# Performance work log

Measured on AMD Instinct MI355X. Metric: run time of the kernel, lower is better.

## Reference

```python
import jax, jax.numpy as jnp
import numpy as np

NUM_HEADS = 16
ROPE_BASE = 10000.0


def _rope_tables(seq_len, head_dim, dtype=jnp.float32):
    # Standard RoPE: inv_freq over even dims, cos/sin of shape [seq, head_dim]
    inv_freq = 1.0 / (ROPE_BASE ** (jnp.arange(0, head_dim, 2, dtype=jnp.float32) / head_dim))
    freqs = jnp.arange(seq_len, dtype=jnp.float32)[:, None] * inv_freq[None, :]  # [S, hd/2]
    emb = jnp.concatenate([freqs, freqs], axis=-1)  # [S, hd]
    return jnp.cos(emb).astype(dtype), jnp.sin(emb).astype(dtype)


def _apply_rope(t, cos, sin):
    # t: [B, H, S, hd]; cos/sin: [S, hd]
    half = t.shape[-1] // 2
    rot = jnp.concatenate([-t[..., half:], t[..., :half]], axis=-1)
    return t * cos[None, None, :, :] + rot * sin[None, None, :, :]


def setup_inputs() -> dict:
    key = jax.random.key(0)
    ks = jax.random.split(key, 7)
    B, S, D, L = 2, 2048, 2048, 256
    sc = lambda fan_in: 1.0 / np.sqrt(fan_in)
    return {
        "x": jax.random.normal(ks[0], (B, S, D), jnp.float32),
        "wq": jax.random.normal(ks[1], (D, D), jnp.float32) * sc(D),
        "wdkv": jax.random.normal(ks[2], (L, D), jnp.float32) * sc(D),
        "wuk": jax.random.normal(ks[3], (D, L), jnp.float32) * sc(L),
        "wuv": jax.random.normal(ks[4], (D, L), jnp.float32) * sc(L),
        "wo": jax.random.normal(ks[5], (D, D), jnp.float32) * sc(D),
        "bo": jnp.zeros((D,), jnp.float32),
    }


def reference(x, wq, wdkv, wuk, wuv, wo, bo):
    B, S, D = x.shape
    H = NUM_HEADS
    hd = wq.shape[0] // H

    # Projections (torch nn.Linear: y = x @ W.T)
    q = jnp.einsum("bsd,ed->bse", x, wq)          # [B, S, D]
    latent = jnp.einsum("bsd,ld->bsl", x, wdkv)   # [B, S, L]
    k = jnp.einsum("bsl,el->bse", latent, wuk)    # [B, S, D]
    v = jnp.einsum("bsl,el->bse", latent, wuv)    # [B, S, D]

    split = lambda t: t.reshape(B, S, H, hd).transpose(0, 2, 1, 3)  # [B, H, S, hd]
    q, k, v = split(q), split(k), split(v)

    cos, sin = _rope_tables(S, hd, x.dtype)
    q = _apply_rope(q, cos, sin)
    k = _apply_rope(k, cos, sin)

    scores = jnp.einsum("bhqd,bhkd->bhqk", q, k) / jnp.sqrt(jnp.asarray(hd, x.dtype))
    causal = jnp.tril(jnp.ones((S, S), bool))
    scores = jnp.where(causal[None, None], scores, jnp.asarray(-jnp.inf, x.dtype))
    attn = jax.nn.softmax(scores, axis=-1)

    ctx = jnp.einsum("bhqk,bhkd->bhqd", attn, v)
    ctx = ctx.transpose(0, 2, 1, 3).reshape(B, S, H * hd)
    return jnp.einsum("bse,oe->bso", ctx, wo) + bo
```

## Files before the change

### kernel.cpp

```cpp
#include <hip/hip_runtime.h>
#include <hip/hip_bf16.h>

typedef __bf16 bf16;
typedef __bf16 bf16x8 __attribute__((ext_vector_type(8)));
typedef __bf16 bf16x4 __attribute__((ext_vector_type(4)));
typedef float  f32x4  __attribute__((ext_vector_type(4)));
typedef float  f32x16 __attribute__((ext_vector_type(16)));
typedef unsigned int u32x4 __attribute__((ext_vector_type(4)));

#define D_MODEL 2048
#define SEQ     2048
#define BATCH   2
#define NHEAD   16
#define HDIM    128
#define LATENT  256
#define BROWS   SEQ

typedef __attribute__((address_space(1))) void gvoid;
typedef __attribute__((address_space(3))) void svoid;

__device__ __forceinline__ void gld16(const bf16* g, bf16* l) {
  __builtin_amdgcn_global_load_lds((gvoid*)(void*)g, (svoid*)l, 16, 0, 0);
}

__device__ __forceinline__ f32x4 mfma16(bf16x8 a, bf16x8 b, f32x4 c) {
  return __builtin_amdgcn_mfma_f32_16x16x32_bf16(a, b, c, 0, 0, 0);
}
__device__ __forceinline__ f32x16 mfma32(bf16x8 a, bf16x8 b, f32x16 c) {
  return __builtin_amdgcn_mfma_f32_32x32x16_bf16(a, b, c, 0, 0, 0);
}

__device__ __forceinline__ unsigned cvt_pk_bf16(float lo, float hi) {
  unsigned r;
  asm("v_cvt_pk_bf16_f32 %0, %1, %2" : "=v"(r) : "v"(lo), "v"(hi));
  return r;
}

__device__ __forceinline__ float fw(float v) {
  union { float f; unsigned u; } x; x.f = v;
  if ((x.u & 0x7f800000u) == 0x7f800000u) return 0.f;
  return v;
}

template<typename T>
__device__ __forceinline__ bf16x8 ld_cvt8(const T* p);
template<>
__device__ __forceinline__ bf16x8 ld_cvt8<float>(const float* p) {
  const float4 a = *(const float4*)p;
  const float4 b = *(const float4*)(p + 4);
  bf16x8 r;
  r[0] = (bf16)a.x; r[1] = (bf16)a.y; r[2] = (bf16)a.z; r[3] = (bf16)a.w;
  r[4] = (bf16)b.x; r[5] = (bf16)b.y; r[6] = (bf16)b.z; r[7] = (bf16)b.w;
  return r;
}
template<>
__device__ __forceinline__ bf16x8 ld_cvt8<bf16>(const bf16* p) {
  return *(const bf16x8*)p;
}

template<typename TC>
__device__ __forceinline__ void st_c(TC* p, float v);
template<> __device__ __forceinline__ void st_c<bf16>(bf16* p, float v)   { *p = (bf16)v; }
template<> __device__ __forceinline__ void st_c<float>(float* p, float v) { *p = v; }

__global__ __launch_bounds__(256)
void cvt_bf16(const float* __restrict__ in, bf16* __restrict__ out, int n8)
{
  int i = blockIdx.x * 256 + threadIdx.x;
  if (i >= n8) return;
  const float4 a = ((const float4*)in)[2 * i];
  const float4 b = ((const float4*)in)[2 * i + 1];
  bf16x8 r;
  r[0] = (bf16)a.x; r[1] = (bf16)a.y; r[2] = (bf16)a.z; r[3] = (bf16)a.w;
  r[4] = (bf16)b.x; r[5] = (bf16)b.y; r[6] = (bf16)b.z; r[7] = (bf16)b.w;
  ((bf16x8*)out)[i] = r;
}

template<typename TA, typename TW, typename TC, int BIAS, int TRANSC>
__global__ __launch_bounds__(256)
void gemm_nt(const TA* __restrict__ A, const TW* __restrict__ W,
             TC* __restrict__ C, const float* __restrict__ bias,
             int M, int N, int K)
{
  const int t    = threadIdx.x;
  const int wave = t >> 6, lane = t & 63;
  const int quad = lane >> 4, l16 = lane & 15;
  const int wr = (wave >> 1) * 64, wc = (wave & 1) * 64;
  const int am0 = blockIdx.x * 128;
  const int bn0 = blockIdx.y * 128;

  __shared__ __align__(16) bf16 As[128][40];
  __shared__ __align__(16) bf16 Bs[128][40];

  const f32x4 fzero = {0.f, 0.f, 0.f, 0.f};
  f32x4 acc[4][4];
#pragma unroll
  for (int i = 0; i < 4; i++)
#pragma unroll
    for (int j = 0; j < 4; j++) acc[i][j] = fzero;

  const int srow = t >> 2;
  const int scol = (t & 3) * 8;

  for (int k0 = 0; k0 < K; k0 += 32) {
#pragma unroll
    for (int c = 0; c < 2; c++) {
      int row = srow + c * 64;
      *(bf16x8*)(&As[row][scol]) =
        ld_cvt8<TA>(A + (size_t)(am0 + row) * K + k0 + scol);
      *(bf16x8*)(&Bs[row][scol]) =
        ld_cvt8<TW>(W + (size_t)(bn0 + row) * K + k0 + scol);
    }
    __syncthreads();

    bf16x8 af[4], bfr[4];
#pragma unroll
    for (int i = 0; i < 4; i++)
      af[i]  = *(const bf16x8*)(&As[wr + i*16 + l16][quad*8]);
#pragma unroll
    for (int j = 0; j < 4; j++)
      bfr[j] = *(const bf16x8*)(&Bs[wc + j*16 + l16][quad*8]);
#pragma unroll
    for (int i = 0; i < 4; i++)
#pragma unroll
      for (int j = 0; j < 4; j++)
        acc[i][j] = mfma16(af[i], bfr[j], acc[i][j]);
    __syncthreads();
  }

#pragma unroll
  for (int i = 0; i < 4; i++) {
#pragma unroll
    for (int j = 0; j < 4; j++) {
      int col = bn0 + wc + j*16 + l16;
      float bv = 0.f;
      if (BIAS) bv = bias[col];
#pragma unroll
      for (int r = 0; r < 4; r++) {
        int row = am0 + wr + i*16 + quad*4 + r;
        if (TRANSC)
          st_c<TC>(&C[(size_t)col * M + row], fw(acc[i][j][r] + bv));
        else
          st_c<TC>(&C[(size_t)row * N + col], fw(acc[i][j][r] + bv));
      }
    }
  }
}

template<typename TC, int BIAS, int TRANSC>
__global__ __launch_bounds__(256)
void gemm_bb(const bf16* __restrict__ A, const bf16* __restrict__ W,
             TC* __restrict__ C, const float* __restrict__ bias,
             int M, int N, int K)
{
  const int t    = threadIdx.x;
  const int wave = t >> 6, lane = t & 63;
  const int quad = lane >> 4, l16 = lane & 15;
  const int wr = (wave >> 1) * 64, wc = (wave & 1) * 64;
  const int am0 = blockIdx.x * 128;
  const int bn0 = blockIdx.y * 128;

  __shared__ __align__(16) bf16 As[128 * 32];
  __shared__ __align__(16) bf16 Bs[128 * 32];

  const f32x4 fzero = {0.f, 0.f, 0.f, 0.f};
  f32x4 acc[4][4];
#pragma unroll
  for (int i = 0; i < 4; i++)
#pragma unroll
    for (int j = 0; j < 4; j++) acc[i][j] = fzero;

  for (int k0 = 0; k0 < K; k0 += 32) {
#pragma unroll
    for (int c = 0; c < 2; c++) {
      int e   = c * 256 + t;
      int row = e >> 2, col = (e & 3) * 8;
      gld16(A + (size_t)(am0 + row) * K + k0 + col, As + e * 8);
      gld16(W + (size_t)(bn0 + row) * K + k0 + col, Bs + e * 8);
    }
    __syncthreads();

    bf16x8 af[4], bfr[4];
#pragma unroll
    for (int i = 0; i < 4; i++)
      af[i]  = *(const bf16x8*)(As + (size_t)(wr + i*16 + l16) * 32 + quad * 8);
#pragma unroll
    for (int j = 0; j < 4; j++)
      bfr[j] = *(const bf16x8*)(Bs + (size_t)(wc + j*16 + l16) * 32 + quad * 8);
#pragma unroll
    for (int i = 0; i < 4; i++)
#pragma unroll
      for (int j = 0; j < 4; j++)
        acc[i][j] = mfma16(af[i], bfr[j], acc[i][j]);
    __syncthreads();
  }

#pragma unroll
  for (int i = 0; i < 4; i++) {
#pragma unroll
    for (int j = 0; j < 4; j++) {
      int col = bn0 + wc + j*16 + l16;
      float bv = 0.f;
      if (BIAS) bv = bias[col];
#pragma unroll
      for (int r = 0; r < 4; r++) {
        int row = am0 + wr + i*16 + quad*4 + r;
        if (TRANSC)
          st_c<TC>(&C[(size_t)col * M + row], fw(acc[i][j][r] + bv));
        else
          st_c<TC>(&C[(size_t)row * N + col], fw(acc[i][j][r] + bv));
      }
    }
  }
}

template<typename TC, int BIAS, int TRANSC>
__global__ __launch_bounds__(256)
void gemm_bf(const bf16* __restrict__ A, const float* __restrict__ W,
             TC* __restrict__ C, const float* __restrict__ bias,
             int M, int N, int K)
{
  const int t    = threadIdx.x;
  const int wave = t >> 6, lane = t & 63;
  const int quad = lane >> 4, l16 = lane & 15;
  const int wr = (wave >> 1) * 64, wc = (wave & 1) * 64;
  const int am0 = blockIdx.x * 128;
  const int bn0 = blockIdx.y * 128;

  __shared__ __align__(16) bf16 As[128 * 32];
  __shared__ __align__(16) bf16 Bs[128][40];

  const f32x4 fzero = {0.f, 0.f, 0.f, 0.f};
  f32x4 acc[4][4];
#pragma unroll
  for (int i = 0; i < 4; i++)
#pragma unroll
    for (int j = 0; j < 4; j++) acc[i][j] = fzero;

  const int srow = t >> 2;
  const int scol = (t & 3) * 8;

  for (int k0 = 0; k0 < K; k0 += 32) {
#pragma unroll
    for (int c = 0; c < 2; c++) {
      int e   = c * 256 + t;
      int row = e >> 2, col = (e & 3) * 8;
      gld16(A + (size_t)(am0 + row) * K + k0 + col, As + e * 8);
      int brow = srow + c * 64;
      *(bf16x8*)(&Bs[brow][scol]) =
        ld_cvt8<float>(W + (size_t)(bn0 + brow) * K + k0 + scol);
    }
    __syncthreads();

    bf16x8 af[4], bfr[4];
#pragma unroll
    for (int i = 0; i < 4; i++)
      af[i]  = *(const bf16x8*)(As + (size_t)(wr + i*16 + l16) * 32 + quad * 8);
#pragma unroll
    for (int j = 0; j < 4; j++)
      bfr[j] = *(const bf16x8*)(&Bs[wc + j*16 + l16][quad*8]);
#pragma unroll
    for (int i = 0; i < 4; i++)
#pragma unroll
      for (int j = 0; j < 4; j++)
        acc[i][j] = mfma16(af[i], bfr[j], acc[i][j]);
    __syncthreads();
  }

#pragma unroll
  for (int i = 0; i < 4; i++) {
#pragma unroll
    for (int j = 0; j < 4; j++) {
      int col = bn0 + wc + j*16 + l16;
      float bv = 0.f;
      if (BIAS) bv = bias[col];
#pragma unroll
      for (int r = 0; r < 4; r++) {
        int row = am0 + wr + i*16 + quad*4 + r;
        if (TRANSC)
          st_c<TC>(&C[(size_t)col * M + row], fw(acc[i][j][r] + bv));
        else
          st_c<TC>(&C[(size_t)row * N + col], fw(acc[i][j][r] + bv));
      }
    }
  }
}

template<int SPLITK>
__global__ __launch_bounds__(256)
void gemm_bf_sk(const bf16* __restrict__ A, const float* __restrict__ W,
                float* __restrict__ Cp, int M, int N, int K)
{
  const int t    = threadIdx.x;
  const int wave = t >> 6, lane = t & 63;
  const int quad = lane >> 4, l16 = lane & 15;
  const int wr = (wave >> 1) * 64, wc = (wave & 1) * 64;
  const int am0 = blockIdx.x * 128;
  const int bn0 = blockIdx.y * 128;
  const int kbeg = blockIdx.z * (K / SPLITK);
  const int kend = kbeg + K / SPLITK;

  __shared__ __align__(16) bf16 As[128 * 32];
  __shared__ __align__(16) bf16 Bs[128][40];

  const f32x4 fzero = {0.f, 0.f, 0.f, 0.f};
  f32x4 acc[4][4];
#pragma unroll
  for (int i = 0; i < 4; i++)
#pragma unroll
    for (int j = 0; j < 4; j++) acc[i][j] = fzero;

  const int srow = t >> 2;
  const int scol = (t & 3) * 8;

  for (int k0 = kbeg; k0 < kend; k0 += 32) {
#pragma unroll
    for (int c = 0; c < 2; c++) {
      int e   = c * 256 + t;
      int row = e >> 2, col = (e & 3) * 8;
      gld16(A + (size_t)(am0 + row) * K + k0 + col, As + e * 8);
      int brow = srow + c * 64;
      *(bf16x8*)(&Bs[brow][scol]) =
        ld_cvt8<float>(W + (size_t)(bn0 + brow) * K + k0 + scol);
    }
    __syncthreads();

    bf16x8 af[4], bfr[4];
#pragma unroll
    for (int i = 0; i < 4; i++)
      af[i]  = *(const bf16x8*)(As + (size_t)(wr + i*16 + l16) * 32 + quad * 8);
#pragma unroll
    for (int j = 0; j < 4; j++)
      bfr[j] = *(const bf16x8*)(&Bs[wc + j*16 + l16][quad*8]);
#pragma unroll
    for (int i = 0; i < 4; i++)
#pragma unroll
      for (int j = 0; j < 4; j++)
        acc[i][j] = mfma16(af[i], bfr[j], acc[i][j]);
    __syncthreads();
  }

  float* Cb = Cp + (size_t)blockIdx.z * M * N;
#pragma unroll
  for (int i = 0; i < 4; i++)
#pragma unroll
    for (int j = 0; j < 4; j++) {
      int col = bn0 + wc + j*16 + l16;
#pragma unroll
      for (int r = 0; r < 4; r++) {
        int row = am0 + wr + i*16 + quad*4 + r;
        Cb[(size_t)row * N + col] = acc[i][j][r];
      }
    }
}

template<int SPLITK>
__global__ __launch_bounds__(256)
void reduce_sk(const float* __restrict__ Cp, bf16* __restrict__ out, int MN)
{
  int i4 = (blockIdx.x * 256 + threadIdx.x) * 4;
  if (i4 >= MN) return;
  float4 s = *(const float4*)(Cp + i4);
#pragma unroll
  for (int k = 1; k < SPLITK; k++) {
    float4 p = *(const float4*)(Cp + (size_t)k * MN + i4);
    s.x += p.x; s.y += p.y; s.z += p.z; s.w += p.w;
  }
  bf16x4 o;
  o[0] = (bf16)fw(s.x); o[1] = (bf16)fw(s.y);
  o[2] = (bf16)fw(s.z); o[3] = (bf16)fw(s.w);
  *(bf16x4*)(out + i4) = o;
}

__global__ __launch_bounds__(256)
void rope_kernel(bf16* __restrict__ Q, bf16* __restrict__ Kr)
{
  int idx = blockIdx.x * 256 + threadIdx.x;
  int j   = idx & 63;
  int h   = (idx >> 6) & 15;
  int row = idx >> 10;
  int s   = row & (SEQ - 1);

  float invf = exp2f(-0.2076205059304601f * (float)j);
  float ang  = (float)s * invf;
  float c = cosf(ang), si = sinf(ang);

  size_t base = (size_t)row * D_MODEL + h * HDIM;
  float q1 = (float)Q[base + j], q2 = (float)Q[base + j + 64];
  Q[base + j]      = (bf16)(q1 * c - q2 * si);
  Q[base + j + 64] = (bf16)(q2 * c + q1 * si);
  float k1 = (float)Kr[base + j], k2 = (float)Kr[base + j + 64];
  Kr[base + j]      = (bf16)(k1 * c - k2 * si);
  Kr[base + j + 64] = (bf16)(k2 * c + k1 * si);
}

__global__ __launch_bounds__(256, 2)
void flash_attn(const bf16* __restrict__ Q, const bf16* __restrict__ Kc,
                const bf16* __restrict__ VT, bf16* __restrict__ O, int ldVT)
{
  const int L    = blockIdx.x;
  const int half = L >> 8;
  const int Mn   = L & 255;
  const int h    = Mn >> 4;
  const int a    = Mn & 15;
  const int qt   = half ? 15 - a : a;
  const int b    = half;
  const int t    = threadIdx.x;
  const int wave = t >> 6, lane = t & 63;
  const int m31  = lane & 31, hi = lane >> 5;
  const int rowbase = b * SEQ;

  __shared__ __align__(16) bf16 Ks[64 * 128];
  __shared__ __align__(16) bf16 Vs[128 * 64];

  bf16x8 qf[8];
  {
    const bf16* qp = Q + (size_t)(rowbase + qt*128 + wave*32 + m31) * D_MODEL
                   + h * HDIM + hi * 8;
#pragma unroll
    for (int dk = 0; dk < 8; dk++)
      qf[dk] = *(const bf16x8*)(qp + dk * 16);
  }

  f32x16 oacc[4];
#pragma unroll
  for (int db = 0; db < 4; db++)
#pragma unroll
    for (int i = 0; i < 16; i++) oacc[db][i] = 0.f;
  float lsum = 0.f;

  const float SC2 = 0.12752051581562927f;

  const int ktmax = 2*qt + 1;
  const bf16* kbase0 = Kc + (size_t)rowbase * D_MODEL + h * HDIM;
  const bf16* vbase0 = VT + (size_t)(h*HDIM) * ldVT + rowbase;

  bf16x8 kr[4], vr[4];
#pragma unroll
  for (int c = 0; c < 4; c++) {
    int e = c*256 + t;
    kr[c] = *(const bf16x8*)(kbase0 + (size_t)(e >> 4) * D_MODEL + (e & 15) * 8);
    vr[c] = *(const bf16x8*)(vbase0 + (size_t)(e >> 3) * ldVT + (e & 7) * 8);
  }

  for (int kt = 0; kt <= ktmax; kt++) {
#pragma unroll
    for (int c = 0; c < 4; c++) {
      int e = c*256 + t;
      int krow = e >> 4, kch = e & 15;
      *(bf16x8*)(Ks + krow * 128 + ((kch ^ (krow & 7)) * 8)) = kr[c];
      int vrow = e >> 3, vch = e & 7;
      *(bf16x8*)(Vs + vrow * 64  + ((vch ^ (vrow & 7)) * 8)) = vr[c];
    }
    __syncthreads();

    if (kt < ktmax) {
      const bf16* kb = kbase0 + (size_t)((kt+1)*64) * D_MODEL;
      const bf16* vb = vbase0 + (kt+1)*64;
#pragma unroll
      for (int c = 0; c < 4; c++) {
        int e = c*256 + t;
        kr[c] = *(const bf16x8*)(kb + (size_t)(e >> 4) * D_MODEL + (e & 15) * 8);
        vr[c] = *(const bf16x8*)(vb + (size_t)(e >> 3) * ldVT + (e & 7) * 8);
      }
    }

    const int kvoff = kt*64 - qt*128;
    const bool activ = (kvoff < 0) | (kvoff <= wave*32 + 31);

    if (activ) {
      unsigned pb[4][4];
#pragma unroll
      for (int kb = 0; kb < 2; kb++) {
        f32x16 s;
#pragma unroll
        for (int i = 0; i < 16; i++) s[i] = 0.f;
        const int krow = kb*32 + m31;
        const bf16* ksrow = Ks + krow * 128;
        const int swz = (krow & 7);
#pragma unroll
        for (int dk = 0; dk < 8; dk++) {
          bf16x8 kf = *(const bf16x8*)(ksrow + (((dk*2 + hi) ^ swz) * 8));
          s = mfma32(kf, qf[dk], s);
        }

        float p[16];
        const int kq = kvoff + kb*32 + 4*hi - (wave*32 + m31);
#pragma unroll
        for (int r = 0; r < 16; r++) {
          float v = s[r] * SC2;
          const int kk = (r & 3) + 8 * (r >> 2);
          if (kvoff >= 0 && (kq + kk) > 0) v = -1e30f;
          float e2 = exp2f(v);
          lsum += e2;
          p[r] = e2;
        }

#pragma unroll
        for (int c = 0; c < 2; c++) {
          unsigned a0 = cvt_pk_bf16(p[(2*c)*4 + 0],   p[(2*c)*4 + 1]);
          unsigned a1 = cvt_pk_bf16(p[(2*c)*4 + 2],   p[(2*c)*4 + 3]);
          unsigned b0 = cvt_pk_bf16(p[(2*c+1)*4 + 0], p[(2*c+1)*4 + 1]);
          unsigned b1 = cvt_pk_bf16(p[(2*c+1)*4 + 2], p[(2*c+1)*4 + 3]);
          asm("v_permlane32_swap_b32 %0, %1" : "+v"(a0), "+v"(b0));
          asm("v_permlane32_swap_b32 %0, %1" : "+v"(a1), "+v"(b1));
          pb[kb*2 + c][0] = a0; pb[kb*2 + c][1] = a1;
          pb[kb*2 + c][2] = b0; pb[kb*2 + c][3] = b1;
        }
      }

#pragma unroll
      for (int db = 0; db < 4; db++) {
        const int vrow = db*32 + m31;
        const bf16* vsrow = Vs + vrow * 64;
        const int swz = (vrow & 7);
#pragma unroll
        for (int kc = 0; kc < 4; kc++) {
          bf16x8 vf = *(const bf16x8*)(vsrow + (((kc*2 + hi) ^ swz) * 8));
          u32x4 w = {pb[kc][0], pb[kc][1], pb[kc][2], pb[kc][3]};
          oacc[db] = mfma32(vf, __builtin_bit_cast(bf16x8, w), oacc[db]);
        }
      }
    }
    __syncthreads();
  }

  const float ltot = lsum + __shfl_xor(lsum, 32, 64);
  const float invl = 1.f / ltot;
  const size_t ob = (size_t)(rowbase + qt*128 + wave*32 + m31) * D_MODEL + h * HDIM;
#pragma unroll
  for (int db = 0; db < 4; db++) {
#pragma unroll
    for (int q2 = 0; q2 < 4; q2++) {
      bf16x4 o4;
#pragma unroll
      for (int rr = 0; rr < 4; rr++)
        o4[rr] = (bf16)(oacc[db][q2*4 + rr] * invl);
      *(bf16x4*)(O + ob + db*32 + q2*8 + hi*4) = o4;
    }
  }
}

extern "C" void kernel_launch(void* const* d_in, const int* in_sizes, int n_in,
                              void* d_out, int out_size, void* d_ws, size_t ws_size,
                              hipStream_t stream)
{
  const float* x    = (const float*)d_in[0];
  const float* wq   = (const float*)d_in[1];
  const float* wdkv = (const float*)d_in[2];
  const float* wuk  = (const float*)d_in[3];
  const float* wuv  = (const float*)d_in[4];
  const float* wo   = (const float*)d_in[5];
  const float* bo   = (const float*)d_in[6];
  float* out = (float*)d_out;

  const size_t MTOT = (size_t)BATCH * BROWS;
  const size_t NEED_FULL = (MTOT * D_MODEL + (size_t)D_MODEL * MTOT
                          + MTOT * LATENT) * sizeof(bf16);

  if (ws_size >= NEED_FULL) {
    bf16* Kb  = (bf16*)d_ws;
    bf16* VTb = Kb  + MTOT * D_MODEL;
    bf16* Lt  = VTb + (size_t)D_MODEL * MTOT;
    bf16* wqb = Kb;
    bf16* wob = VTb;
    float* Pp = (float*)d_ws;
    bf16* sb  = (bf16*)out;
    bf16* xb  = sb + MTOT * D_MODEL;

    cvt_bf16<<<(int)(MTOT * D_MODEL / 8 / 256), 256, 0, stream>>>(x,  xb,  (int)(MTOT * D_MODEL / 8));
    cvt_bf16<<<(int)((size_t)D_MODEL * D_MODEL / 8 / 256), 256, 0, stream>>>(wq, wqb, (int)((size_t)D_MODEL * D_MODEL / 8));

    gemm_bb<bf16, 0, 0><<<dim3(32, 16), 256, 0, stream>>>(xb, wqb, sb, nullptr, (int)MTOT, D_MODEL, D_MODEL);

    gemm_bf_sk<8><<<dim3(32, 2, 8), 256, 0, stream>>>(xb, wdkv, Pp, (int)MTOT, LATENT, D_MODEL);
    reduce_sk<8><<<(int)(MTOT * LATENT / 4 / 256), 256, 0, stream>>>(Pp, Lt, (int)(MTOT * LATENT));
    gemm_bf<bf16, 0, 0><<<dim3(32, 16), 256, 0, stream>>>(Lt, wuk,  Kb,  nullptr, (int)MTOT, D_MODEL, LATENT);
    gemm_bf<bf16, 0, 1><<<dim3(32, 16), 256, 0, stream>>>(Lt, wuv,  VTb, nullptr, (int)MTOT, D_MODEL, LATENT);

    rope_kernel<<<(int)(MTOT * NHEAD * 64) / 256, 256, 0, stream>>>(sb, Kb);

    flash_attn<<<dim3(512), 256, 0, stream>>>(sb, Kb, VTb, sb, (int)MTOT);

    cvt_bf16<<<(int)((size_t)D_MODEL * D_MODEL / 8 / 256), 256, 0, stream>>>(wo, wob, (int)((size_t)D_MODEL * D_MODEL / 8));
    hipMemcpyAsync(Kb, sb, MTOT * D_MODEL * sizeof(bf16),
                   hipMemcpyDeviceToDevice, stream);

    gemm_bb<float, 1, 0><<<dim3(32, 16), 256, 0, stream>>>(Kb, wob, out, bo, (int)MTOT, D_MODEL, D_MODEL);
  } else {
    bf16* Kb  = (bf16*)d_ws;
    bf16* VTb = Kb + (size_t)BROWS * D_MODEL;

    for (int b = 0; b < BATCH; b++) {
      const float* xb   = x   + (size_t)b * BROWS * D_MODEL;
      float*       outb = out + (size_t)b * BROWS * D_MODEL;
      bf16*        sb   = (bf16*)outb;

      gemm_nt<float, float, bf16, 0, 0><<<dim3(16, 2),  256, 0, stream>>>(xb, wdkv, sb,  nullptr, BROWS, LATENT,  D_MODEL);
      gemm_nt<bf16,  float, bf16, 0, 0><<<dim3(16, 16), 256, 0, stream>>>(sb, wuk,  Kb,  nullptr, BROWS, D_MODEL, LATENT);
      gemm_nt<bf16,  float, bf16, 0, 1><<<dim3(16, 16), 256, 0, stream>>>(sb, wuv,  VTb, nullptr, BROWS, D_MODEL, LATENT);
      gemm_nt<float, float, bf16, 0, 0><<<dim3(16, 16), 256, 0, stream>>>(xb, wq,   sb,  nullptr, BROWS, D_MODEL, D_MODEL);

      rope_kernel<<<(BROWS * NHEAD * 64) / 256, 256, 0, stream>>>(sb, Kb);

      flash_attn<<<dim3(256), 256, 0, stream>>>(sb, Kb, VTb, sb, BROWS);

      hipMemcpyAsync(Kb, sb, (size_t)BROWS * D_MODEL * sizeof(bf16),
                     hipMemcpyDeviceToDevice, stream);
      gemm_nt<bf16, float, float, 1, 0><<<dim3(16, 16), 256, 0, stream>>>(Kb, wo, outb, bo, BROWS, D_MODEL, D_MODEL);
    }
  }
}
```

Measured before the change: 373.5 us.

## Fuse input conversions, vectorize RoPE and transposed stores, tune attention scheduling

Merges the x and wq fp32-to-bf16 conversions into one launch and vectorizes the RoPE kernel to 8-element loads and stores with sincosf. The transposed GEMM epilogue now writes bf16x4 packets instead of scalars. In attention, block-to-(head, query tile) mapping is swapped, s_setprio brackets the MFMA loops, and the row-sum accumulator is split four ways to shorten the dependency chain. The aim is to cut launch count, memory transactions and scheduling stalls, at the cost of more per-thread RoPE work and a changed tile ordering that may affect cache reuse.

```diff
diff --git a/kernel.cpp b/kernel.cpp
--- a/kernel.cpp
+++ b/kernel.cpp
@@ -76,6 +76,26 @@
   ((bf16x8*)out)[i] = r;
 }
 
+__global__ __launch_bounds__(256)
+void cvt2_bf16(const float* __restrict__ inA, bf16* __restrict__ outA, int n8A,
+               const float* __restrict__ inB, bf16* __restrict__ outB, int n8B)
+{
+  int i = blockIdx.x * 256 + threadIdx.x;
+  const float* in; bf16* out; int k;
+  if (i < n8A) { in = inA; out = outA; k = i; }
+  else {
+    k = i - n8A;
+    if (k >= n8B) return;
+    in = inB; out = outB;
+  }
+  const float4 a = ((const float4*)in)[2 * k];
+  const float4 b = ((const float4*)in)[2 * k + 1];
+  bf16x8 r;
+  r[0] = (bf16)a.x; r[1] = (bf16)a.y; r[2] = (bf16)a.z; r[3] = (bf16)a.w;
+  r[4] = (bf16)b.x; r[5] = (bf16)b.y; r[6] = (bf16)b.z; r[7] = (bf16)b.w;
+  ((bf16x8*)out)[k] = r;
+}
+
 template<typename TA, typename TW, typename TC, int BIAS, int TRANSC>
 __global__ __launch_bounds__(256)
 void gemm_nt(const TA* __restrict__ A, const TW* __restrict__ W,
@@ -274,13 +294,16 @@
       int col = bn0 + wc + j*16 + l16;
       float bv = 0.f;
       if (BIAS) bv = bias[col];
-#pragma unroll
-      for (int r = 0; r < 4; r++) {
-        int row = am0 + wr + i*16 + quad*4 + r;
-        if (TRANSC)
-          st_c<TC>(&C[(size_t)col * M + row], fw(acc[i][j][r] + bv));
-        else
-          st_c<TC>(&C[(size_t)row * N + col], fw(acc[i][j][r] + bv));
+      int row0 = am0 + wr + i*16 + quad*4;
+      if (TRANSC) {
+        bf16x4 o4;
+#pragma unroll
+        for (int r = 0; r < 4; r++) o4[r] = (bf16)fw(acc[i][j][r] + bv);
+        *(bf16x4*)((bf16*)C + (size_t)col * M + row0) = o4;
+      } else {
+#pragma unroll
+        for (int r = 0; r < 4; r++)
+          st_c<TC>(&C[(size_t)(row0 + r) * N + col], fw(acc[i][j][r] + bv));
       }
     }
   }
@@ -376,22 +399,35 @@
 void rope_kernel(bf16* __restrict__ Q, bf16* __restrict__ Kr)
 {
   int idx = blockIdx.x * 256 + threadIdx.x;
-  int j   = idx & 63;
-  int h   = (idx >> 6) & 15;
-  int row = idx >> 10;
+  int jg  = idx & 7;
+  int h   = (idx >> 3) & 15;
+  int row = idx >> 7;
   int s   = row & (SEQ - 1);
 
-  float invf = exp2f(-0.2076205059304601f * (float)j);
-  float ang  = (float)s * invf;
-  float c = cosf(ang), si = sinf(ang);
-
-  size_t base = (size_t)row * D_MODEL + h * HDIM;
-  float q1 = (float)Q[base + j], q2 = (float)Q[base + j + 64];
-  Q[base + j]      = (bf16)(q1 * c - q2 * si);
-  Q[base + j + 64] = (bf16)(q2 * c + q1 * si);
-  float k1 = (float)Kr[base + j], k2 = (float)Kr[base + j + 64];
-  Kr[base + j]      = (bf16)(k1 * c - k2 * si);
-  Kr[base + j + 64] = (bf16)(k2 * c + k1 * si);
+  size_t base = (size_t)row * D_MODEL + h * HDIM + jg * 8;
+  bf16x8 q1 = *(const bf16x8*)(Q  + base);
+  bf16x8 q2 = *(const bf16x8*)(Q  + base + 64);
+  bf16x8 k1 = *(const bf16x8*)(Kr + base);
+  bf16x8 k2 = *(const bf16x8*)(Kr + base + 64);
+  bf16x8 q1o, q2o, k1o, k2o;
+#pragma unroll
+  for (int u = 0; u < 8; u++) {
+    int j = jg * 8 + u;
+    float invf = exp2f(-0.2076205059304601f * (float)j);
+    float ang  = (float)s * invf;
+    float c, si;
+    sincosf(ang, &si, &c);
+    float a1 = (float)q1[u], a2 = (float)q2[u];
+    q1o[u] = (bf16)(a1 * c - a2 * si);
+    q2o[u] = (bf16)(a2 * c + a1 * si);
+    float b1 = (float)k1[u], b2 = (float)k2[u];
+    k1o[u] = (bf16)(b1 * c - b2 * si);
+    k2o[u] = (bf16)(b2 * c + b1 * si);
+  }
+  *(bf16x8*)(Q  + base)      = q1o;
+  *(bf16x8*)(Q  + base + 64) = q2o;
+  *(bf16x8*)(Kr + base)      = k1o;
+  *(bf16x8*)(Kr + base + 64) = k2o;
 }
 
 __global__ __launch_bounds__(256, 2)
@@ -401,8 +437,8 @@
   const int L    = blockIdx.x;
   const int half = L >> 8;
   const int Mn   = L & 255;
-  const int h    = Mn >> 4;
-  const int a    = Mn & 15;
+  const int h    = Mn & 15;
+  const int a    = Mn >> 4;
   const int qt   = half ? 15 - a : a;
   const int b    = half;
   const int t    = threadIdx.x;
@@ -427,7 +463,7 @@
   for (int db = 0; db < 4; db++)
 #pragma unroll
     for (int i = 0; i < 16; i++) oacc[db][i] = 0.f;
-  float lsum = 0.f;
+  float ls[4] = {0.f, 0.f, 0.f, 0.f};
 
   const float SC2 = 0.12752051581562927f;
 
@@ -478,11 +514,13 @@
         const int krow = kb*32 + m31;
         const bf16* ksrow = Ks + krow * 128;
         const int swz = (krow & 7);
+        __builtin_amdgcn_s_setprio(1);
 #pragma unroll
         for (int dk = 0; dk < 8; dk++) {
           bf16x8 kf = *(const bf16x8*)(ksrow + (((dk*2 + hi) ^ swz) * 8));
           s = mfma32(kf, qf[dk], s);
         }
+        __builtin_amdgcn_s_setprio(0);
 
         float p[16];
         const int kq = kvoff + kb*32 + 4*hi - (wave*32 + m31);
@@ -492,7 +530,7 @@
           const int kk = (r & 3) + 8 * (r >> 2);
           if (kvoff >= 0 && (kq + kk) > 0) v = -1e30f;
           float e2 = exp2f(v);
-          lsum += e2;
+          ls[r & 3] += e2;
           p[r] = e2;
         }
 
@@ -509,6 +547,7 @@
         }
       }
 
+      __builtin_amdgcn_s_setprio(1);
 #pragma unroll
       for (int db = 0; db < 4; db++) {
         const int vrow = db*32 + m31;
@@ -521,10 +560,12 @@
           oacc[db] = mfma32(vf, __builtin_bit_cast(bf16x8, w), oacc[db]);
         }
       }
-    }
-    __syncthreads();
-  }
-
+      __builtin_amdgcn_s_setprio(0);
+    }
+    __syncthreads();
+  }
+
+  const float lsum = (ls[0] + ls[1]) + (ls[2] + ls[3]);
   const float ltot = lsum + __shfl_xor(lsum, 32, 64);
   const float invl = 1.f / ltot;
   const size_t ob = (size_t)(rowbase + qt*128 + wave*32 + m31) * D_MODEL + h * HDIM;
@@ -568,8 +609,10 @@
     bf16* sb  = (bf16*)out;
     bf16* xb  = sb + MTOT * D_MODEL;
 
-    cvt_bf16<<<(int)(MTOT * D_MODEL / 8 / 256), 256, 0, stream>>>(x,  xb,  (int)(MTOT * D_MODEL / 8));
-    cvt_bf16<<<(int)((size_t)D_MODEL * D_MODEL / 8 / 256), 256, 0, stream>>>(wq, wqb, (int)((size_t)D_MODEL * D_MODEL / 8));
+    const int n8x = (int)(MTOT * D_MODEL / 8);
+    const int n8w = (int)((size_t)D_MODEL * D_MODEL / 8);
+
+    cvt2_bf16<<<(n8x + n8w) / 256, 256, 0, stream>>>(x, xb, n8x, wq, wqb, n8w);
 
     gemm_bb<bf16, 0, 0><<<dim3(32, 16), 256, 0, stream>>>(xb, wqb, sb, nullptr, (int)MTOT, D_MODEL, D_MODEL);
 
@@ -578,11 +621,11 @@
     gemm_bf<bf16, 0, 0><<<dim3(32, 16), 256, 0, stream>>>(Lt, wuk,  Kb,  nullptr, (int)MTOT, D_MODEL, LATENT);
     gemm_bf<bf16, 0, 1><<<dim3(32, 16), 256, 0, stream>>>(Lt, wuv,  VTb, nullptr, (int)MTOT, D_MODEL, LATENT);
 
-    rope_kernel<<<(int)(MTOT * NHEAD * 64) / 256, 256, 0, stream>>>(sb, Kb);
+    rope_kernel<<<(int)(MTOT * NHEAD * 8) / 256, 256, 0, stream>>>(sb, Kb);
 
     flash_attn<<<dim3(512), 256, 0, stream>>>(sb, Kb, VTb, sb, (int)MTOT);
 
-    cvt_bf16<<<(int)((size_t)D_MODEL * D_MODEL / 8 / 256), 256, 0, stream>>>(wo, wob, (int)((size_t)D_MODEL * D_MODEL / 8));
+    cvt_bf16<<<n8w / 256, 256, 0, stream>>>(wo, wob, n8w);
     hipMemcpyAsync(Kb, sb, MTOT * D_MODEL * sizeof(bf16),
                    hipMemcpyDeviceToDevice, stream);
 
@@ -601,7 +644,7 @@
       gemm_nt<bf16,  float, bf16, 0, 1><<<dim3(16, 16), 256, 0, stream>>>(sb, wuv,  VTb, nullptr, BROWS, D_MODEL, LATENT);
       gemm_nt<float, float, bf16, 0, 0><<<dim3(16, 16), 256, 0, stream>>>(xb, wq,   sb,  nullptr, BROWS, D_MODEL, D_MODEL);
 
-      rope_kernel<<<(BROWS * NHEAD * 64) / 256, 256, 0, stream>>>(sb, Kb);
+      rope_kernel<<<(BROWS * NHEAD * 8) / 256, 256, 0, stream>>>(sb, Kb);
 
       flash_attn<<<dim3(256), 256, 0, stream>>>(sb, Kb, VTb, sb, BROWS);
 
```

After: 376.3 us. About the same (+0.8%).
